# Kernel optimization log

Hardware: AMD Instinct MI355X
Metric: run time of the kernel (lower is better)

## Reference

```python
import jax, jax.numpy as jnp
import numpy as np

B, N, D, H, C = 16, 512, 256, 8, 16
DK = D // H  # per-head dim


def gelu(x):
    return jax.nn.gelu(x, approximate=False)  # torch F.gelu default (erf)


def mha(x, Wq, Wk, Wv, Wo):
    # x: [N, D] treated as a length-N token sequence; standard scaled-dot MHA
    n = x.shape[0]
    q = (x @ Wq).reshape(n, H, DK)
    k = (x @ Wk).reshape(n, H, DK)
    v = (x @ Wv).reshape(n, H, DK)
    scores = jnp.einsum('nhd,mhd->hnm', q, k) / jnp.sqrt(jnp.asarray(DK, x.dtype))
    attn = jax.nn.softmax(scores, axis=-1)
    out = jnp.einsum('hnm,mhd->nhd', attn, v).reshape(n, H * DK)
    return out @ Wo


def setup_inputs() -> dict:
    key = jax.random.key(0)
    ks = jax.random.split(key, 16)
    scale = 1.0 / np.sqrt(D)
    w = lambda i, shape: jax.random.normal(ks[i], shape, jnp.float32) * scale
    return {
        'embeddings': jax.random.normal(ks[0], (B, N, D), jnp.float32),
        'labels': jax.random.randint(ks[1], (B, N), 0, C),
        'Wq0': w(2, (D, D)), 'Wk0': w(3, (D, D)), 'Wv0': w(4, (D, D)), 'Wo0': w(5, (D, D)),
        'Wq1': w(6, (D, D)), 'Wk1': w(7, (D, D)), 'Wv1': w(8, (D, D)), 'Wo1': w(9, (D, D)),
        'res_W': w(10, (D, D)), 'res_b': jnp.zeros((D,), jnp.float32),
        'ff_W1': w(11, (2 * D, D)), 'ff_b1': jnp.zeros((D,), jnp.float32),
        'ff_W2': w(12, (D, D)), 'ff_b2': jnp.zeros((D,), jnp.float32),
    }


def reference(embeddings, labels, Wq0, Wk0, Wv0, Wo0, Wq1, Wk1, Wv1, Wo1,
              res_W, res_b, ff_W1, ff_b1, ff_W2, ff_b2):
    # one-hot class membership; torch.unique over randint labels == arange(C)
    onehot = (labels[..., None] == jnp.arange(C)).astype(jnp.float32)  # [B,N,C]

    def episode(e, m):
        # e: [N, D]  m: [N, C]
        x = mha(e, Wq0, Wk0, Wv0, Wo0)
        x = gelu(x)
        x = mha(x, Wq1, Wk1, Wv1, Wo1)
        aggr = gelu(jnp.mean(x, axis=0))          # [D]  set-level summary
        aggr = aggr @ res_W + res_b               # res_linear
        e2 = jnp.concatenate([jnp.broadcast_to(aggr, (N, D)), e], axis=1)  # [N,2D]
        e2 = gelu(e2)
        e2 = gelu(e2 @ ff_W1 + ff_b1) @ ff_W2 + ff_b2  # ff_linear -> [N,D]
        # pairwise sample similarities with self-exclusion
        S = e2 @ e2.T                              # [N,N]
        S = S * (1.0 - jnp.eye(N, dtype=S.dtype))
        counts = jnp.sum(m, axis=0)                # [C]
        norm = counts[None, :] - m                 # leave-one-out class size [N,C]
        return (S.T @ m) / norm                    # per-class masked mean -> [N,C]

    return jax.vmap(episode)(embeddings, onehot)
```

## Files before the change

### kernel.cpp

```cpp
#include <hip/hip_runtime.h>

#define BB 16
#define NN 512
#define DD 256
#define HH 8
#define CC 16

typedef unsigned short u16;
using short8 = __attribute__((ext_vector_type(8))) short;
using f32x4  = __attribute__((ext_vector_type(4))) float;

__device__ __forceinline__ float gelu_f(float x) {
    return 0.5f * x * (1.0f + erff(x * 0.70710678118654752f));
}
__device__ __forceinline__ u16 f2bf(float f) {
    unsigned int u = __float_as_uint(f);
    unsigned int r = u + 0x7FFFu + ((u >> 16) & 1u);
    return (u16)(r >> 16);
}
__device__ __forceinline__ void gld16(const u16* g, const u16* l) {
    __builtin_amdgcn_global_load_lds(
        (const __attribute__((address_space(1))) unsigned int*)g,
        (__attribute__((address_space(3))) unsigned int*)l, 16, 0, 0);
}

#define QSCALE 0.25505412f

template<int ACT, int HAS_B, int HAS_T, int OUT_F32, int QKV>
__global__ __launch_bounds__(256) void gemm64(
    const u16* __restrict__ A,
    const u16* __restrict__ W0, const u16* __restrict__ W1, const u16* __restrict__ W2,
    u16* __restrict__ O0, u16* __restrict__ O1, u16* __restrict__ O2,
    float* __restrict__ OF,
    const float* __restrict__ bias, const float* __restrict__ tvec)
{
    __shared__ __align__(16) u16 As[64 * 32];
    __shared__ __align__(16) u16 Bs[64 * 32];
    const int tid = threadIdx.x, wave = tid >> 6, lane = tid & 63;
    const int col = lane & 15, quad = lane >> 4;
    const int mbase = blockIdx.x * 64;
    int sel, nbase;
    if (QKV) { sel = blockIdx.y >> 2; nbase = (blockIdx.y & 3) * 64; }
    else     { sel = 0;               nbase = blockIdx.y * 64; }
    const u16* W = (sel == 0) ? W0 : ((sel == 1) ? W1 : W2);
    u16* O = (sel == 0) ? O0 : ((sel == 1) ? O1 : O2);
    const int srow = lane >> 2, skk = (lane & 3) * 8;
    const int mh = (wave & 1) * 32, nh = (wave >> 1) * 32;

    f32x4 acc[2][2];
#pragma unroll
    for (int i = 0; i < 2; ++i)
#pragma unroll
        for (int j = 0; j < 2; ++j) acc[i][j] = (f32x4){0.f, 0.f, 0.f, 0.f};

    for (int k0 = 0; k0 < DD; k0 += 32) {
        gld16(A + (size_t)(mbase + wave * 16 + srow) * DD + k0 + skk, &As[wave * 512]);
        gld16(W + (size_t)(nbase + wave * 16 + srow) * DD + k0 + skk, &Bs[wave * 512]);
        __syncthreads();
        short8 af[2], bfr[2];
#pragma unroll
        for (int i = 0; i < 2; ++i) af[i]  = *(const short8*)&As[(mh + i * 16 + col) * 32 + quad * 8];
#pragma unroll
        for (int j = 0; j < 2; ++j) bfr[j] = *(const short8*)&Bs[(nh + j * 16 + col) * 32 + quad * 8];
#pragma unroll
        for (int i = 0; i < 2; ++i)
#pragma unroll
            for (int j = 0; j < 2; ++j)
                acc[i][j] = __builtin_amdgcn_mfma_f32_16x16x32_bf16(af[i], bfr[j], acc[i][j], 0, 0, 0);
        __syncthreads();
    }

    const int b = mbase >> 9;
#pragma unroll
    for (int i = 0; i < 2; ++i) {
#pragma unroll
        for (int j = 0; j < 2; ++j) {
            const int ccol = nbase + nh + j * 16 + col;
            const int tok0 = (mbase & 511) + mh + i * 16 + quad * 4;
            if (QKV) {
                const int head = ccol >> 5, dk = ccol & 31;
                if (sel == 2) {
                    ushort4 pk;
                    pk.x = f2bf(acc[i][j][0]); pk.y = f2bf(acc[i][j][1]);
                    pk.z = f2bf(acc[i][j][2]); pk.w = f2bf(acc[i][j][3]);
                    *(ushort4*)&O[(((size_t)b * HH + head) * 32 + dk) * NN + tok0] = pk;
                } else {
#pragma unroll
                    for (int r = 0; r < 4; ++r) {
                        float v = acc[i][j][r];
                        if (sel == 0) v *= QSCALE;
                        O[(((size_t)b * HH + head) * NN + tok0 + r) * 32 + dk] = f2bf(v);
                    }
                }
            } else {
#pragma unroll
                for (int r = 0; r < 4; ++r) {
                    const int crow = mbase + mh + i * 16 + quad * 4 + r;
                    float v = acc[i][j][r];
                    if (HAS_B) v += bias[ccol];
                    if (HAS_T) v += tvec[b * DD + ccol];
                    if (ACT)   v = gelu_f(v);
                    if (OUT_F32) OF[(size_t)crow * DD + ccol] = v;
                    else         O[(size_t)crow * DD + ccol] = f2bf(v);
                }
            }
        }
    }
}

template<int COLSUM>
__global__ __launch_bounds__(256) void attn_mfma(
    const u16* __restrict__ Qh, const u16* __restrict__ Kh,
    const u16* __restrict__ VT, u16* __restrict__ O,
    float* __restrict__ partial)
{
    __shared__ __align__(16) u16 Vt[32 * 520];
    __shared__ __align__(16) u16 Pc[4][16 * 32];
    __shared__ float cs[4][32];
    const int tid = threadIdx.x, wave = tid >> 6, lane = tid & 63;
    const int col = lane & 15, quad = lane >> 4;
    const int gid = blockIdx.x;
    const int qb = gid >> 7, bh = gid & 127;
    const int q0 = qb * 64 + wave * 16;

    const u16* vsrc = VT + (size_t)bh * 32 * NN;
#pragma unroll
    for (int i = 0; i < 8; ++i) {
        const int row = wave + i * 4;
        gld16(vsrc + (size_t)row * NN + lane * 8, &Vt[row * 520]);
    }
    const short8 aq = *(const short8*)(Qh + ((size_t)bh * NN + q0 + col) * 32 + quad * 8);
    __syncthreads();

    const u16* ksrc = Kh + (size_t)bh * NN * 32;
    float l[4] = {0.f, 0.f, 0.f, 0.f};
    f32x4 oacc[2];
    oacc[0] = (f32x4){0.f, 0.f, 0.f, 0.f};
    oacc[1] = (f32x4){0.f, 0.f, 0.f, 0.f};

    for (int g = 0; g < 16; ++g) {
#pragma unroll
        for (int k2 = 0; k2 < 2; ++k2) {
            const int kt = g * 2 + k2;
            const short8 bk = *(const short8*)(ksrc + (size_t)(kt * 16 + col) * 32 + quad * 8);
            f32x4 z = {0.f, 0.f, 0.f, 0.f};
            const f32x4 s = __builtin_amdgcn_mfma_f32_16x16x32_bf16(aq, bk, z, 0, 0, 0);
#pragma unroll
            for (int r = 0; r < 4; ++r) {
                const float p = exp2f(s[r]);
                l[r] += p;
                Pc[wave][(quad * 4 + r) * 32 + k2 * 16 + col] = f2bf(p);
            }
        }
        const short8 ap = *(const short8*)&Pc[wave][col * 32 + quad * 8];
#pragma unroll
        for (int nt = 0; nt < 2; ++nt) {
            const short8 bv = *(const short8*)&Vt[(nt * 16 + col) * 520 + g * 32 + quad * 8];
            oacc[nt] = __builtin_amdgcn_mfma_f32_16x16x32_bf16(ap, bv, oacc[nt], 0, 0, 0);
        }
    }
#pragma unroll
    for (int r = 0; r < 4; ++r) {
        l[r] += __shfl_xor(l[r], 1, 64);
        l[r] += __shfl_xor(l[r], 2, 64);
        l[r] += __shfl_xor(l[r], 4, 64);
        l[r] += __shfl_xor(l[r], 8, 64);
    }
    if (COLSUM) {
        float sv[2] = {0.f, 0.f};
#pragma unroll
        for (int nt = 0; nt < 2; ++nt) {
#pragma unroll
            for (int r = 0; r < 4; ++r) sv[nt] += oacc[nt][r] / l[r];
            sv[nt] += __shfl_xor(sv[nt], 16, 64);
            sv[nt] += __shfl_xor(sv[nt], 32, 64);
        }
        if (lane < 16) { cs[wave][col] = sv[0]; cs[wave][16 + col] = sv[1]; }
        __syncthreads();
        if (tid < 32)
            partial[(size_t)(bh * 8 + qb) * 32 + tid] =
                cs[0][tid] + cs[1][tid] + cs[2][tid] + cs[3][tid];
    } else {
        const int b = bh >> 3, h = bh & 7;
        u16* obase = O + ((size_t)b * NN) * DD + h * 32;
#pragma unroll
        for (int nt = 0; nt < 2; ++nt)
#pragma unroll
            for (int r = 0; r < 4; ++r)
                obase[(size_t)(q0 + quad * 4 + r) * DD + nt * 16 + col] = f2bf(oacc[nt][r] / l[r]);
    }
}

__global__ __launch_bounds__(256) void convert_all(
    const float* __restrict__ e, u16* __restrict__ E, u16* __restrict__ G,
    const float* s0, const float* s1, const float* s2, const float* s3,
    const float* s4, const float* s5, const float* s6, const float* s7,
    const float* s8, u16* __restrict__ Wt)
{
    const int bx = blockIdx.x;
    if (bx < 2048) {
        const size_t i = ((size_t)bx * 256 + threadIdx.x) * 4;
        const float4 v = *(const float4*)(e + i);
        ushort4 ev, gv;
        ev.x = f2bf(v.x); ev.y = f2bf(v.y); ev.z = f2bf(v.z); ev.w = f2bf(v.w);
        gv.x = f2bf(gelu_f(v.x)); gv.y = f2bf(gelu_f(v.y));
        gv.z = f2bf(gelu_f(v.z)); gv.w = f2bf(gelu_f(v.w));
        *(ushort4*)(E + i) = ev;
        *(ushort4*)(G + i) = gv;
    } else {
        const int w = bx - 2048;
        const int my = w >> 4, kb = (w & 15) * 16;
        const int n = threadIdx.x;
        const float* S;
        switch (my) {
            case 0: S = s0; break; case 1: S = s1; break; case 2: S = s2; break;
            case 3: S = s3; break; case 4: S = s4; break; case 5: S = s5; break;
            case 6: S = s6; break; case 7: S = s7; break; default: S = s8; break;
        }
        u16* Dst = Wt + (size_t)my * 65536;
        for (int r = 0; r < 16; ++r) {
            const int k = kb + r;
            Dst[(size_t)n * 256 + k] = f2bf(S[(size_t)k * 256 + n]);
        }
    }
}

__global__ __launch_bounds__(256) void aggr_kernel(
    const float* __restrict__ partial, const float* __restrict__ Wo1f,
    const float* __restrict__ resW, const float* __restrict__ resb,
    const float* __restrict__ W1, float* __restrict__ tvec)
{
    const int b = blockIdx.x, d = threadIdx.x;
    __shared__ float a0[256], a1[256], a2[256];
    const int h = d >> 5, d32 = d & 31;
    float s = 0.f;
#pragma unroll
    for (int qb = 0; qb < 8; ++qb)
        s += partial[(size_t)(((b * 8 + h) * 8) + qb) * 32 + d32];
    a0[d] = s * (1.0f / NN);
    __syncthreads();
    float y = 0.f;
    for (int k = 0; k < 256; ++k) y += a0[k] * Wo1f[(size_t)k * 256 + d];
    a1[d] = gelu_f(y);
    __syncthreads();
    float t = resb[d];
    for (int k = 0; k < 256; ++k) t += a1[k] * resW[(size_t)k * 256 + d];
    a2[d] = gelu_f(t);
    __syncthreads();
    float u = 0.f;
    for (int k = 0; k < 256; ++k) u += a2[k] * W1[(size_t)k * 256 + d];
    tvec[b * 256 + d] = u;
}

__global__ __launch_bounds__(256) void classsum_kernel(
    const float* __restrict__ F, const int* __restrict__ labels,
    float* __restrict__ g, float* __restrict__ counts)
{
    const int b = blockIdx.x, dch = blockIdx.y;
    const int t = threadIdx.x, w = t >> 6, lane = t & 63;
    __shared__ int lab[NN];
    __shared__ float gs[4][CC][64];
    lab[t] = labels[b * NN + t];
    lab[t + 256] = labels[b * NN + t + 256];
#pragma unroll
    for (int c = 0; c < CC; ++c) gs[w][c][lane] = 0.f;
    __syncthreads();
    const float* Fb = F + (size_t)b * NN * DD + dch * 64;
    for (int n = w * 128; n < w * 128 + 128; ++n)
        gs[w][lab[n]][lane] += Fb[(size_t)n * DD + lane];
    __syncthreads();
#pragma unroll
    for (int i = 0; i < 4; ++i) {
        const int c = w * 4 + i;
        const float v = gs[0][c][lane] + gs[1][c][lane] + gs[2][c][lane] + gs[3][c][lane];
        g[((size_t)b * CC + c) * DD + dch * 64 + lane] = v;
    }
    if (dch == 0 && t < CC) {
        int cnt = 0;
        for (int n = 0; n < NN; ++n) cnt += (lab[n] == t);
        counts[b * CC + t] = (float)cnt;
    }
}

__global__ __launch_bounds__(256) void out_kernel(
    const float* __restrict__ F, const int* __restrict__ labels,
    const float* __restrict__ g, const float* __restrict__ counts,
    float* __restrict__ out)
{
    const int b = blockIdx.y;
    const int wave = threadIdx.x >> 6, lane = threadIdx.x & 63;
    const int n = blockIdx.x * 4 + wave;
    const float* fn = F + ((size_t)b * NN + n) * DD;
    const float* gb = g + (size_t)b * CC * DD;
    float fv[4];
#pragma unroll
    for (int i = 0; i < 4; ++i) fv[i] = fn[lane * 4 + i];
    float selfdot = 0.f;
#pragma unroll
    for (int i = 0; i < 4; ++i) selfdot += fv[i] * fv[i];
    float accs[CC];
#pragma unroll
    for (int c = 0; c < CC; ++c) {
        float sacc = 0.f;
#pragma unroll
        for (int i = 0; i < 4; ++i) sacc += fv[i] * gb[c * DD + lane * 4 + i];
        accs[c] = sacc;
    }
    for (int off = 32; off; off >>= 1) {
        selfdot += __shfl_xor(selfdot, off, 64);
#pragma unroll
        for (int c = 0; c < CC; ++c) accs[c] += __shfl_xor(accs[c], off, 64);
    }
    if (lane < CC) {
        const int c = lane;
        const int same = (labels[b * NN + n] == c) ? 1 : 0;
        const float num = accs[c] - (same ? selfdot : 0.f);
        const float den = counts[b * CC + c] - (float)same;
        out[((size_t)b * NN + n) * CC + c] = num / den;
    }
}

extern "C" void kernel_launch(void* const* d_in, const int* in_sizes, int n_in,
                              void* d_out, int out_size, void* d_ws, size_t ws_size,
                              hipStream_t stream)
{
    const float* emb    = (const float*)d_in[0];
    const int*   labels = (const int*)  d_in[1];
    const float* Wo1f = (const float*)d_in[9];
    const float* resW = (const float*)d_in[10];
    const float* resb = (const float*)d_in[11];
    const float* ffW1 = (const float*)d_in[12];
    const float* ffb1 = (const float*)d_in[13];
    const float* ffb2 = (const float*)d_in[15];
    float* out = (float*)d_out;

    const size_t SBE = (size_t)BB * NN * DD;
    u16* BUF0 = (u16*)d_ws;
    u16* BUF1 = BUF0 + SBE;
    u16* BUF2 = BUF1 + SBE;
    u16* BUF3 = BUF2 + SBE;
    u16* BUF4 = BUF3 + SBE;
    u16* BUF5 = BUF4 + SBE;
    u16* Wt   = BUF5 + SBE;
    float* F      = (float*)(Wt + 9 * 65536);
    float* tvec   = F + SBE;
    float* partial= tvec + BB * 256;
    float* gsum   = partial + 128 * 8 * 32;
    float* counts = gsum + (size_t)BB * CC * DD;

    convert_all<<<2048 + 144, 256, 0, stream>>>(
        emb, BUF0, BUF1,
        (const float*)d_in[2], (const float*)d_in[3], (const float*)d_in[4],
        (const float*)d_in[5], (const float*)d_in[6], (const float*)d_in[7],
        (const float*)d_in[8], ffW1 + 256 * 256, (const float*)d_in[14], Wt);
    gemm64<0,0,0,0,1><<<dim3(128, 12), 256, 0, stream>>>(
        BUF0, Wt, Wt + 65536, Wt + 2 * 65536, BUF2, BUF3, BUF4, nullptr, nullptr, nullptr);
    attn_mfma<0><<<1024, 256, 0, stream>>>(BUF2, BUF3, BUF4, BUF5, nullptr);
    gemm64<1,0,0,0,0><<<dim3(128, 4), 256, 0, stream>>>(
        BUF5, Wt + 3 * 65536, nullptr, nullptr, BUF0, nullptr, nullptr, nullptr, nullptr, nullptr);
    gemm64<0,0,0,0,1><<<dim3(128, 12), 256, 0, stream>>>(
        BUF0, Wt + 4 * 65536, Wt + 5 * 65536, Wt + 6 * 65536, BUF2, BUF3, BUF4, nullptr, nullptr, nullptr);
    attn_mfma<1><<<1024, 256, 0, stream>>>(BUF2, BUF3, BUF4, nullptr, partial);
    aggr_kernel<<<BB, 256, 0, stream>>>(partial, Wo1f, resW, resb, ffW1, tvec);
    gemm64<1,1,1,0,0><<<dim3(128, 4), 256, 0, stream>>>(
        BUF1, Wt + 7 * 65536, nullptr, nullptr, BUF3, nullptr, nullptr, nullptr, ffb1, tvec);
    gemm64<0,1,0,1,0><<<dim3(128, 4), 256, 0, stream>>>(
        BUF3, Wt + 8 * 65536, nullptr, nullptr, nullptr, nullptr, nullptr, F, ffb2, nullptr);
    classsum_kernel<<<dim3(BB, 4), 256, 0, stream>>>(F, labels, gsum, counts);
    out_kernel<<<dim3(128, BB), 256, 0, stream>>>(F, labels, gsum, counts, out);
}
```

Before: 211.7 us.

## Fuse back-to-back GEMM chains into per-row-tile kernels and streamline small kernels

Fuses the Wo0 projection, GELU and the three layer-1 QKV projections into one kernel that keeps the 64x256 GELU tile in LDS. The two feed-forward GEMMs are fused the same way, so those intermediates no longer round-trip through global memory and two launches go away. Class counts move into the aggregation kernel via an LDS histogram. The class-sum kernel switches to register accumulation, and the matvecs use 8-way split accumulators. In exchange, the fused kernels launch only 128 blocks, which is fewer than the CU count. They also read weights directly from global memory without LDS staging, which may leave the GPU underutilized.

```diff
diff --git a/kernel.cpp b/kernel.cpp
--- a/kernel.cpp
+++ b/kernel.cpp
@@ -26,22 +26,18 @@
 
 #define QSCALE 0.25505412f
 
-template<int ACT, int HAS_B, int HAS_T, int OUT_F32, int QKV>
-__global__ __launch_bounds__(256) void gemm64(
+__global__ __launch_bounds__(256) void gemm_qkv(
     const u16* __restrict__ A,
     const u16* __restrict__ W0, const u16* __restrict__ W1, const u16* __restrict__ W2,
-    u16* __restrict__ O0, u16* __restrict__ O1, u16* __restrict__ O2,
-    float* __restrict__ OF,
-    const float* __restrict__ bias, const float* __restrict__ tvec)
+    u16* __restrict__ O0, u16* __restrict__ O1, u16* __restrict__ O2)
 {
     __shared__ __align__(16) u16 As[64 * 32];
     __shared__ __align__(16) u16 Bs[64 * 32];
     const int tid = threadIdx.x, wave = tid >> 6, lane = tid & 63;
     const int col = lane & 15, quad = lane >> 4;
     const int mbase = blockIdx.x * 64;
-    int sel, nbase;
-    if (QKV) { sel = blockIdx.y >> 2; nbase = (blockIdx.y & 3) * 64; }
-    else     { sel = 0;               nbase = blockIdx.y * 64; }
+    const int sel = blockIdx.y >> 2;
+    const int nbase = (blockIdx.y & 3) * 64;
     const u16* W = (sel == 0) ? W0 : ((sel == 1) ? W1 : W2);
     u16* O = (sel == 0) ? O0 : ((sel == 1) ? O1 : O2);
     const int srow = lane >> 2, skk = (lane & 3) * 8;
@@ -77,31 +73,18 @@
         for (int j = 0; j < 2; ++j) {
             const int ccol = nbase + nh + j * 16 + col;
             const int tok0 = (mbase & 511) + mh + i * 16 + quad * 4;
-            if (QKV) {
-                const int head = ccol >> 5, dk = ccol & 31;
-                if (sel == 2) {
-                    ushort4 pk;
-                    pk.x = f2bf(acc[i][j][0]); pk.y = f2bf(acc[i][j][1]);
-                    pk.z = f2bf(acc[i][j][2]); pk.w = f2bf(acc[i][j][3]);
-                    *(ushort4*)&O[(((size_t)b * HH + head) * 32 + dk) * NN + tok0] = pk;
-                } else {
-#pragma unroll
-                    for (int r = 0; r < 4; ++r) {
-                        float v = acc[i][j][r];
-                        if (sel == 0) v *= QSCALE;
-                        O[(((size_t)b * HH + head) * NN + tok0 + r) * 32 + dk] = f2bf(v);
-                    }
-                }
+            const int head = ccol >> 5, dk = ccol & 31;
+            if (sel == 2) {
+                ushort4 pk;
+                pk.x = f2bf(acc[i][j][0]); pk.y = f2bf(acc[i][j][1]);
+                pk.z = f2bf(acc[i][j][2]); pk.w = f2bf(acc[i][j][3]);
+                *(ushort4*)&O[(((size_t)b * HH + head) * 32 + dk) * NN + tok0] = pk;
             } else {
 #pragma unroll
                 for (int r = 0; r < 4; ++r) {
-                    const int crow = mbase + mh + i * 16 + quad * 4 + r;
                     float v = acc[i][j][r];
-                    if (HAS_B) v += bias[ccol];
-                    if (HAS_T) v += tvec[b * DD + ccol];
-                    if (ACT)   v = gelu_f(v);
-                    if (OUT_F32) OF[(size_t)crow * DD + ccol] = v;
-                    else         O[(size_t)crow * DD + ccol] = f2bf(v);
+                    if (sel == 0) v *= QSCALE;
+                    O[(((size_t)b * HH + head) * NN + tok0 + r) * 32 + dk] = f2bf(v);
                 }
             }
         }
@@ -188,6 +171,213 @@
 #pragma unroll
             for (int r = 0; r < 4; ++r)
                 obase[(size_t)(q0 + quad * 4 + r) * DD + nt * 16 + col] = f2bf(oacc[nt][r] / l[r]);
+    }
+}
+
+__global__ __launch_bounds__(256) void fused_x1qkv1(
+    const u16* __restrict__ A5, const u16* __restrict__ Wo0t,
+    const u16* __restrict__ Wq1t, const u16* __restrict__ Wk1t,
+    const u16* __restrict__ Wv1t,
+    u16* __restrict__ Qh, u16* __restrict__ Kh, u16* __restrict__ VT)
+{
+    __shared__ __align__(16) u16 T32[8][64][40];
+    const int tid = threadIdx.x, wave = tid >> 6, lane = tid & 63;
+    const int col = lane & 15, quad = lane >> 4;
+    const int mbase = blockIdx.x * 64, b = blockIdx.x >> 3;
+    const int mh = (wave & 1) * 32, nh = (wave >> 1) * 32;
+
+    {
+        f32x4 acc[4][2][2];
+#pragma unroll
+        for (int nt = 0; nt < 4; ++nt)
+#pragma unroll
+            for (int i = 0; i < 2; ++i)
+#pragma unroll
+                for (int j = 0; j < 2; ++j) acc[nt][i][j] = (f32x4){0.f, 0.f, 0.f, 0.f};
+        for (int kc = 0; kc < 8; ++kc) {
+            short8 af[2];
+#pragma unroll
+            for (int i = 0; i < 2; ++i)
+                af[i] = *(const short8*)(A5 + (size_t)(mbase + mh + i * 16 + col) * DD + kc * 32 + quad * 8);
+#pragma unroll
+            for (int nt = 0; nt < 4; ++nt) {
+                short8 bfr[2];
+#pragma unroll
+                for (int j = 0; j < 2; ++j)
+                    bfr[j] = *(const short8*)(Wo0t + (size_t)(nt * 64 + nh + j * 16 + col) * DD + kc * 32 + quad * 8);
+#pragma unroll
+                for (int i = 0; i < 2; ++i)
+#pragma unroll
+                    for (int j = 0; j < 2; ++j)
+                        acc[nt][i][j] = __builtin_amdgcn_mfma_f32_16x16x32_bf16(af[i], bfr[j], acc[nt][i][j], 0, 0, 0);
+            }
+        }
+#pragma unroll
+        for (int nt = 0; nt < 4; ++nt)
+#pragma unroll
+            for (int i = 0; i < 2; ++i)
+#pragma unroll
+                for (int j = 0; j < 2; ++j) {
+                    const int ccol = nt * 64 + nh + j * 16 + col;
+#pragma unroll
+                    for (int r = 0; r < 4; ++r) {
+                        const int row = mh + i * 16 + quad * 4 + r;
+                        T32[ccol >> 5][row][ccol & 31] = f2bf(gelu_f(acc[nt][i][j][r]));
+                    }
+                }
+    }
+    __syncthreads();
+
+    const u16* Ws[3] = {Wq1t, Wk1t, Wv1t};
+    for (int sel = 0; sel < 3; ++sel) {
+        const u16* W = Ws[sel];
+        f32x4 acc[4][2][2];
+#pragma unroll
+        for (int nt = 0; nt < 4; ++nt)
+#pragma unroll
+            for (int i = 0; i < 2; ++i)
+#pragma unroll
+                for (int j = 0; j < 2; ++j) acc[nt][i][j] = (f32x4){0.f, 0.f, 0.f, 0.f};
+        for (int kc = 0; kc < 8; ++kc) {
+            short8 af[2];
+#pragma unroll
+            for (int i = 0; i < 2; ++i)
+                af[i] = *(const short8*)&T32[kc][mh + i * 16 + col][quad * 8];
+#pragma unroll
+            for (int nt = 0; nt < 4; ++nt) {
+                short8 bfr[2];
+#pragma unroll
+                for (int j = 0; j < 2; ++j)
+                    bfr[j] = *(const short8*)(W + (size_t)(nt * 64 + nh + j * 16 + col) * DD + kc * 32 + quad * 8);
+#pragma unroll
+                for (int i = 0; i < 2; ++i)
+#pragma unroll
+                    for (int j = 0; j < 2; ++j)
+                        acc[nt][i][j] = __builtin_amdgcn_mfma_f32_16x16x32_bf16(af[i], bfr[j], acc[nt][i][j], 0, 0, 0);
+            }
+        }
+#pragma unroll
+        for (int nt = 0; nt < 4; ++nt)
+#pragma unroll
+            for (int i = 0; i < 2; ++i)
+#pragma unroll
+                for (int j = 0; j < 2; ++j) {
+                    const int ccol = nt * 64 + nh + j * 16 + col;
+                    const int head = ccol >> 5, dk = ccol & 31;
+                    const int tok0 = (mbase & 511) + mh + i * 16 + quad * 4;
+                    if (sel == 2) {
+                        ushort4 pk;
+                        pk.x = f2bf(acc[nt][i][j][0]); pk.y = f2bf(acc[nt][i][j][1]);
+                        pk.z = f2bf(acc[nt][i][j][2]); pk.w = f2bf(acc[nt][i][j][3]);
+                        *(ushort4*)&VT[(((size_t)b * HH + head) * 32 + dk) * NN + tok0] = pk;
+                    } else {
+                        u16* O = (sel == 0) ? Qh : Kh;
+#pragma unroll
+                        for (int r = 0; r < 4; ++r) {
+                            float v = acc[nt][i][j][r];
+                            if (sel == 0) v *= QSCALE;
+                            O[(((size_t)b * HH + head) * NN + tok0 + r) * 32 + dk] = f2bf(v);
+                        }
+                    }
+                }
+    }
+}
+
+__global__ __launch_bounds__(256) void fused_hf(
+    const u16* __restrict__ G, const u16* __restrict__ W1t,
+    const u16* __restrict__ W2t, const float* __restrict__ b1,
+    const float* __restrict__ tvec, const float* __restrict__ b2,
+    float* __restrict__ OF)
+{
+    __shared__ __align__(16) u16 T32[8][64][40];
+    const int tid = threadIdx.x, wave = tid >> 6, lane = tid & 63;
+    const int col = lane & 15, quad = lane >> 4;
+    const int mbase = blockIdx.x * 64, b = blockIdx.x >> 3;
+    const int mh = (wave & 1) * 32, nh = (wave >> 1) * 32;
+
+    {
+        f32x4 acc[4][2][2];
+#pragma unroll
+        for (int nt = 0; nt < 4; ++nt)
+#pragma unroll
+            for (int i = 0; i < 2; ++i)
+#pragma unroll
+                for (int j = 0; j < 2; ++j) acc[nt][i][j] = (f32x4){0.f, 0.f, 0.f, 0.f};
+        for (int kc = 0; kc < 8; ++kc) {
+            short8 af[2];
+#pragma unroll
+            for (int i = 0; i < 2; ++i)
+                af[i] = *(const short8*)(G + (size_t)(mbase + mh + i * 16 + col) * DD + kc * 32 + quad * 8);
+#pragma unroll
+            for (int nt = 0; nt < 4; ++nt) {
+                short8 bfr[2];
+#pragma unroll
+                for (int j = 0; j < 2; ++j)
+                    bfr[j] = *(const short8*)(W1t + (size_t)(nt * 64 + nh + j * 16 + col) * DD + kc * 32 + quad * 8);
+#pragma unroll
+                for (int i = 0; i < 2; ++i)
+#pragma unroll
+                    for (int j = 0; j < 2; ++j)
+                        acc[nt][i][j] = __builtin_amdgcn_mfma_f32_16x16x32_bf16(af[i], bfr[j], acc[nt][i][j], 0, 0, 0);
+            }
+        }
+#pragma unroll
+        for (int nt = 0; nt < 4; ++nt)
+#pragma unroll
+            for (int i = 0; i < 2; ++i)
+#pragma unroll
+                for (int j = 0; j < 2; ++j) {
+                    const int ccol = nt * 64 + nh + j * 16 + col;
+                    const float add = b1[ccol] + tvec[b * DD + ccol];
+#pragma unroll
+                    for (int r = 0; r < 4; ++r) {
+                        const int row = mh + i * 16 + quad * 4 + r;
+                        T32[ccol >> 5][row][ccol & 31] = f2bf(gelu_f(acc[nt][i][j][r] + add));
+                    }
+                }
+    }
+    __syncthreads();
+
+    {
+        f32x4 acc[4][2][2];
+#pragma unroll
+        for (int nt = 0; nt < 4; ++nt)
+#pragma unroll
+            for (int i = 0; i < 2; ++i)
+#pragma unroll
+                for (int j = 0; j < 2; ++j) acc[nt][i][j] = (f32x4){0.f, 0.f, 0.f, 0.f};
+        for (int kc = 0; kc < 8; ++kc) {
+            short8 af[2];
+#pragma unroll
+            for (int i = 0; i < 2; ++i)
+                af[i] = *(const short8*)&T32[kc][mh + i * 16 + col][quad * 8];
+#pragma unroll
+            for (int nt = 0; nt < 4; ++nt) {
+                short8 bfr[2];
+#pragma unroll
+                for (int j = 0; j < 2; ++j)
+                    bfr[j] = *(const short8*)(W2t + (size_t)(nt * 64 + nh + j * 16 + col) * DD + kc * 32 + quad * 8);
+#pragma unroll
+                for (int i = 0; i < 2; ++i)
+#pragma unroll
+                    for (int j = 0; j < 2; ++j)
+                        acc[nt][i][j] = __builtin_amdgcn_mfma_f32_16x16x32_bf16(af[i], bfr[j], acc[nt][i][j], 0, 0, 0);
+            }
+        }
+#pragma unroll
+        for (int nt = 0; nt < 4; ++nt)
+#pragma unroll
+            for (int i = 0; i < 2; ++i)
+#pragma unroll
+                for (int j = 0; j < 2; ++j) {
+                    const int ccol = nt * 64 + nh + j * 16 + col;
+                    const float bb = b2[ccol];
+#pragma unroll
+                    for (int r = 0; r < 4; ++r) {
+                        const int crow = mbase + mh + i * 16 + quad * 4 + r;
+                        OF[(size_t)crow * DD + ccol] = acc[nt][i][j][r] + bb;
+                    }
+                }
     }
 }
 
@@ -225,13 +415,28 @@
     }
 }
 
-__global__ __launch_bounds__(256) void aggr_kernel(
+__device__ __forceinline__ float mv256(const float* __restrict__ a,
+                                       const float* __restrict__ W, int d)
+{
+    float acc[8] = {0.f, 0.f, 0.f, 0.f, 0.f, 0.f, 0.f, 0.f};
+    for (int k = 0; k < 256; k += 8) {
+#pragma unroll
+        for (int j = 0; j < 8; ++j)
+            acc[j] += a[k + j] * W[(size_t)(k + j) * 256 + d];
+    }
+    return ((acc[0] + acc[1]) + (acc[2] + acc[3])) + ((acc[4] + acc[5]) + (acc[6] + acc[7]));
+}
+
+__global__ __launch_bounds__(256) void aggr_v2(
     const float* __restrict__ partial, const float* __restrict__ Wo1f,
     const float* __restrict__ resW, const float* __restrict__ resb,
-    const float* __restrict__ W1, float* __restrict__ tvec)
+    const float* __restrict__ W1, const int* __restrict__ labels,
+    float* __restrict__ tvec, float* __restrict__ counts)
 {
     const int b = blockIdx.x, d = threadIdx.x;
     __shared__ float a0[256], a1[256], a2[256];
+    __shared__ int hist[CC];
+    if (d < CC) hist[d] = 0;
     const int h = d >> 5, d32 = d & 31;
     float s = 0.f;
 #pragma unroll
@@ -239,22 +444,19 @@
         s += partial[(size_t)(((b * 8 + h) * 8) + qb) * 32 + d32];
     a0[d] = s * (1.0f / NN);
     __syncthreads();
-    float y = 0.f;
-    for (int k = 0; k < 256; ++k) y += a0[k] * Wo1f[(size_t)k * 256 + d];
-    a1[d] = gelu_f(y);
-    __syncthreads();
-    float t = resb[d];
-    for (int k = 0; k < 256; ++k) t += a1[k] * resW[(size_t)k * 256 + d];
-    a2[d] = gelu_f(t);
-    __syncthreads();
-    float u = 0.f;
-    for (int k = 0; k < 256; ++k) u += a2[k] * W1[(size_t)k * 256 + d];
-    tvec[b * 256 + d] = u;
-}
-
-__global__ __launch_bounds__(256) void classsum_kernel(
+    atomicAdd(&hist[labels[b * NN + d]], 1);
+    atomicAdd(&hist[labels[b * NN + 256 + d]], 1);
+    a1[d] = gelu_f(mv256(a0, Wo1f, d));
+    __syncthreads();
+    a2[d] = gelu_f(mv256(a1, resW, d) + resb[d]);
+    __syncthreads();
+    tvec[b * 256 + d] = mv256(a2, W1, d);
+    if (d < CC) counts[b * CC + d] = (float)hist[d];
+}
+
+__global__ __launch_bounds__(256) void classsum_v2(
     const float* __restrict__ F, const int* __restrict__ labels,
-    float* __restrict__ g, float* __restrict__ counts)
+    float* __restrict__ g)
 {
     const int b = blockIdx.x, dch = blockIdx.y;
     const int t = threadIdx.x, w = t >> 6, lane = t & 63;
@@ -262,23 +464,26 @@
     __shared__ float gs[4][CC][64];
     lab[t] = labels[b * NN + t];
     lab[t + 256] = labels[b * NN + t + 256];
-#pragma unroll
-    for (int c = 0; c < CC; ++c) gs[w][c][lane] = 0.f;
-    __syncthreads();
-    const float* Fb = F + (size_t)b * NN * DD + dch * 64;
-    for (int n = w * 128; n < w * 128 + 128; ++n)
-        gs[w][lab[n]][lane] += Fb[(size_t)n * DD + lane];
+    __syncthreads();
+    float acc[CC];
+#pragma unroll
+    for (int c = 0; c < CC; ++c) acc[c] = 0.f;
+    const float* Fb = F + (size_t)b * NN * DD + dch * 64 + lane;
+#pragma unroll 4
+    for (int n = w * 128; n < w * 128 + 128; ++n) {
+        const float v = Fb[(size_t)n * DD];
+        const int lb = lab[n];
+#pragma unroll
+        for (int c = 0; c < CC; ++c) acc[c] += (lb == c) ? v : 0.f;
+    }
+#pragma unroll
+    for (int c = 0; c < CC; ++c) gs[w][c][lane] = acc[c];
     __syncthreads();
 #pragma unroll
     for (int i = 0; i < 4; ++i) {
         const int c = w * 4 + i;
-        const float v = gs[0][c][lane] + gs[1][c][lane] + gs[2][c][lane] + gs[3][c][lane];
-        g[((size_t)b * CC + c) * DD + dch * 64 + lane] = v;
-    }
-    if (dch == 0 && t < CC) {
-        int cnt = 0;
-        for (int n = 0; n < NN; ++n) cnt += (lab[n] == t);
-        counts[b * CC + t] = (float)cnt;
+        g[((size_t)b * CC + c) * DD + dch * 64 + lane] =
+            gs[0][c][lane] + gs[1][c][lane] + gs[2][c][lane] + gs[3][c][lane];
     }
 }
 
@@ -353,19 +558,16 @@
         (const float*)d_in[2], (const float*)d_in[3], (const float*)d_in[4],
         (const float*)d_in[5], (const float*)d_in[6], (const float*)d_in[7],
         (const float*)d_in[8], ffW1 + 256 * 256, (const float*)d_in[14], Wt);
-    gemm64<0,0,0,0,1><<<dim3(128, 12), 256, 0, stream>>>(
-        BUF0, Wt, Wt + 65536, Wt + 2 * 65536, BUF2, BUF3, BUF4, nullptr, nullptr, nullptr);
+    gemm_qkv<<<dim3(128, 12), 256, 0, stream>>>(
+        BUF0, Wt, Wt + 65536, Wt + 2 * 65536, BUF2, BUF3, BUF4);
     attn_mfma<0><<<1024, 256, 0, stream>>>(BUF2, BUF3, BUF4, BUF5, nullptr);
-    gemm64<1,0,0,0,0><<<dim3(128, 4), 256, 0, stream>>>(
-        BUF5, Wt + 3 * 65536, nullptr, nullptr, BUF0, nullptr, nullptr, nullptr, nullptr, nullptr);
-    gemm64<0,0,0,0,1><<<dim3(128, 12), 256, 0, stream>>>(
-        BUF0, Wt + 4 * 65536, Wt + 5 * 65536, Wt + 6 * 65536, BUF2, BUF3, BUF4, nullptr, nullptr, nullptr);
+    fused_x1qkv1<<<128, 256, 0, stream>>>(
+        BUF5, Wt + 3 * 65536, Wt + 4 * 65536, Wt + 5 * 65536, Wt + 6 * 65536,
+        BUF2, BUF3, BUF4);
     attn_mfma<1><<<1024, 256, 0, stream>>>(BUF2, BUF3, BUF4, nullptr, partial);
-    aggr_kernel<<<BB, 256, 0, stream>>>(partial, Wo1f, resW, resb, ffW1, tvec);
-    gemm64<1,1,1,0,0><<<dim3(128, 4), 256, 0, stream>>>(
-        BUF1, Wt + 7 * 65536, nullptr, nullptr, BUF3, nullptr, nullptr, nullptr, ffb1, tvec);
-    gemm64<0,1,0,1,0><<<dim3(128, 4), 256, 0, stream>>>(
-        BUF3, Wt + 8 * 65536, nullptr, nullptr, nullptr, nullptr, nullptr, F, ffb2, nullptr);
-    classsum_kernel<<<dim3(BB, 4), 256, 0, stream>>>(F, labels, gsum, counts);
+    aggr_v2<<<BB, 256, 0, stream>>>(partial, Wo1f, resW, resb, ffW1, labels, tvec, counts);
+    fused_hf<<<128, 256, 0, stream>>>(
+        BUF1, Wt + 7 * 65536, Wt + 8 * 65536, ffb1, tvec, ffb2, F);
+    classsum_v2<<<dim3(BB, 4), 256, 0, stream>>>(F, labels, gsum);
     out_kernel<<<dim3(128, BB), 256, 0, stream>>>(F, labels, gsum, counts, out);
 }
```

New measurement: 264.0 us. 1.25x slower.
